# Kernel tuning notes

Measured on AMD Instinct MI355X. Metric: run time of the kernel, lower is better.

Reference implementation:

```python
import jax, jax.numpy as jnp
import numpy as np

ENTITY_TOTAL = 100000
RELATION_TOTAL = 500
NUM_RELATIONS = 2 * RELATION_TOTAL  # 1000
DIM = 128
NUM_BASES = 4
NUM_EDGES = 600000


def setup_inputs() -> dict:
    key = jax.random.key(0)
    ks = jax.random.split(key, 16)
    d = {}
    d['entity'] = jnp.arange(ENTITY_TOTAL, dtype=jnp.int64 if jax.config.jax_enable_x64 else jnp.int32)
    d['edge_index'] = jax.random.randint(ks[0], (2, NUM_EDGES), 0, ENTITY_TOTAL)
    d['edge_type'] = jax.random.randint(ks[1], (NUM_EDGES,), 0, NUM_RELATIONS)
    d['edge_norm'] = jax.random.uniform(ks[2], (NUM_EDGES,), dtype=jnp.float32)
    d['DAD_rel'] = jax.random.normal(ks[3], (RELATION_TOTAL, RELATION_TOTAL), dtype=jnp.float32)
    # learned parameters
    d['entity_table'] = jax.random.normal(ks[4], (ENTITY_TOTAL, DIM), dtype=jnp.float32)
    d['relation_emb'] = jax.random.normal(ks[5], (RELATION_TOTAL, DIM), dtype=jnp.float32) * (6.0 / (RELATION_TOTAL + DIM)) ** 0.5
    def rgcn_params(k):
        k1, k2, k3 = jax.random.split(k, 3)
        basis = jax.random.normal(k1, (NUM_BASES, DIM, DIM), dtype=jnp.float32) / np.sqrt(DIM)
        att = jax.random.normal(k2, (NUM_RELATIONS, NUM_BASES), dtype=jnp.float32) / np.sqrt(NUM_BASES)
        root = jax.random.normal(k3, (DIM, DIM), dtype=jnp.float32) / np.sqrt(DIM)
        bias = jnp.zeros((DIM,), dtype=jnp.float32)
        return basis, att, root, bias
    d['basis1'], d['att1'], d['root1'], d['bias1'] = rgcn_params(ks[6])
    d['basis2'], d['att2'], d['root2'], d['bias2'] = rgcn_params(ks[7])
    return d


def rgcn_conv(x, edge_index, edge_type, edge_norm, basis, att, root, bias):
    # PyG-style basis-decomposed RGCNConv, aggr='mean', source_to_target flow.
    num_nodes = x.shape[0]
    src, dst = edge_index[0], edge_index[1]
    x_j = x[src]                     # [E, in] gather
    att_e = att[edge_type]           # [E, B]
    # per-edge relation transform: sum_b att_e[:,b] * (x_j @ basis[b]); loop over
    # NUM_BASES (=4) avoids materializing [E, in, out].
    msg = jnp.zeros((x_j.shape[0], basis.shape[2]), dtype=x.dtype)
    for b in range(basis.shape[0]):
        msg = msg + att_e[:, b:b + 1] * (x_j @ basis[b])
    msg = msg * edge_norm[:, None]
    agg = jax.ops.segment_sum(msg, dst, num_segments=num_nodes)
    deg = jax.ops.segment_sum(jnp.ones_like(edge_norm), dst, num_segments=num_nodes)
    agg = agg / jnp.maximum(deg, 1.0)[:, None]   # mean aggregation
    return agg + x @ root + bias


def reference(entity, edge_index, edge_type, edge_norm, DAD_rel,
              entity_table, relation_emb,
              basis1, att1, root1, bias1,
              basis2, att2, root2, bias2):
    h = entity_table[entity]  # embedding lookup [N, dim]
    h = jax.nn.relu(rgcn_conv(h, edge_index, edge_type, edge_norm, basis1, att1, root1, bias1))
    # dropout(p=0.2) is identity in eval mode (deterministic reference)
    h = rgcn_conv(h, edge_index, edge_type, edge_norm, basis2, att2, root2, bias2)
    return (h, relation_emb)
```

## Files before the change

kernel.cpp:

```cpp
#include <hip/hip_runtime.h>
#include <hip/hip_bf16.h>

#define NROWS 100000
#define EDGES 600000
#define DIM 128
#define SCAN_B 391

typedef unsigned short u16;
typedef __attribute__((ext_vector_type(8))) short v8s;
typedef __attribute__((ext_vector_type(4))) float v4f;
typedef __attribute__((ext_vector_type(2))) float f2;

static __device__ __forceinline__ float bf2f(u16 u) {
  union { unsigned u; float f; } c;
  c.u = (unsigned)u << 16;
  return c.f;
}
static __device__ __forceinline__ u16 f2bf(float f) {
  union { float f; unsigned u; } c;
  c.f = f;
  unsigned r = c.u + 0x7fff + ((c.u >> 16) & 1);
  return (u16)(r >> 16);
}
static __device__ __forceinline__ f2 bfpair(unsigned v) {
  union { unsigned u[2]; f2 f; } c;
  c.u[0] = v << 16;
  c.u[1] = v & 0xffff0000u;
  return c.f;
}
static __device__ __forceinline__ long ld_idx(const void* p, long i, int is64) {
  return is64 ? (long)((const long long*)p)[i] : (long)((const int*)p)[i];
}
static __device__ __forceinline__ float ld_f(const int* flags, const void* p, long i) {
  return flags[0] ? ((const float*)p)[i] : bf2f(((const u16*)p)[i]);
}

__global__ __launch_bounds__(256) void detect_kernel(
    const u16* __restrict__ table, const void* __restrict__ entity,
    const void* __restrict__ ei, const void* __restrict__ et,
    int* __restrict__ flags) {
  int gid = blockIdx.x * 256 + threadIdx.x;
  const ushort4* t4 = (const ushort4*)table;
  ushort4 v = t4[gid];
  int cf = ((((v.x >> 7) & 0xFF) == 0xFF) ? 1 : 0) +
           ((((v.y >> 7) & 0xFF) == 0xFF) ? 1 : 0) +
           ((((v.z >> 7) & 0xFF) == 0xFF) ? 1 : 0) +
           ((((v.w >> 7) & 0xFF) == 0xFF) ? 1 : 0);
  int cei = 0, cet = 0;
  if (gid < 1024) {
    cei = (((const int*)ei)[2 * gid + 1] != 0) ? 1 : 0;
    cet = (((const int*)et)[2 * gid + 1] != 0) ? 1 : 0;
  }
  __shared__ int s_f, s_ei, s_et;
  if (threadIdx.x == 0) { s_f = 0; s_ei = 0; s_et = 0; }
  __syncthreads();
  if (cf) atomicAdd(&s_f, cf);
  if (cei) atomicAdd(&s_ei, cei);
  if (cet) atomicAdd(&s_et, cet);
  __syncthreads();
  if (threadIdx.x == 0) {
    if (s_f) atomicAdd(flags + 0, s_f);
    if (s_ei) atomicAdd(flags + 2, s_ei);
    if (s_et) atomicAdd(flags + 3, s_et);
  }
  if (gid == 0) flags[1] = (((const int*)entity)[1] == 0) ? 1 : 0;
}

__global__ __launch_bounds__(256) void prep_kernel(
    const int* __restrict__ flags,
    const void* __restrict__ basis0, const void* __restrict__ root0, u16* __restrict__ Wt0,
    const void* __restrict__ basis1, const void* __restrict__ root1, u16* __restrict__ Wt1,
    const void* __restrict__ att0, const void* __restrict__ att1,
    float* __restrict__ attf0, float* __restrict__ attf1,
    const void* __restrict__ bias0, const void* __restrict__ bias1,
    float* __restrict__ biasf0, float* __restrict__ biasf1,
    const void* __restrict__ rel, float* __restrict__ relout) {
  int i = blockIdx.x * 256 + threadIdx.x;
  if (i < 2 * 81920) {
    const void* basis = (i < 81920) ? basis0 : basis1;
    const void* root = (i < 81920) ? root0 : root1;
    u16* Wt = (i < 81920) ? Wt0 : Wt1;
    int j = (i < 81920) ? i : i - 81920;
    int n = j >> 7, k = j & 127;
    float v;
    if (n < 512) {
      int b = n >> 7, c = n & 127;
      v = ld_f(flags, basis, (long)b * DIM * DIM + (long)k * DIM + c);
    } else {
      v = ld_f(flags, root, (long)k * DIM + (n - 512));
    }
    Wt[j] = f2bf(v);
    return;
  }
  i -= 163840;
  if (i < 64000) { relout[i] = ld_f(flags, rel, i); return; }
  i -= 64000;
  if (i < 4000) { attf0[i] = ld_f(flags, att0, i); return; }
  i -= 4000;
  if (i < 4000) { attf1[i] = ld_f(flags, att1, i); return; }
  i -= 4000;
  if (i < 128) { biasf0[i] = ld_f(flags, bias0, i); return; }
  i -= 128;
  if (i < 128) biasf1[i] = ld_f(flags, bias1, i);
}
#define PREP_THREADS (163840 + 64000 + 4000 + 4000 + 128 + 128)

__global__ __launch_bounds__(256) void gather_kernel(const int* __restrict__ flags,
                                                     const void* __restrict__ entity,
                                                     const void* __restrict__ table,
                                                     u16* __restrict__ hbf) {
  int gid = blockIdx.x * 256 + threadIdx.x;
  int row = gid >> 5, c4 = (gid & 31) * 4;
  if (row >= NROWS) return;
  long src = ld_idx(entity, row, flags[1]);
  ushort4 o;
  if (flags[0]) {
    float4 a = *(const float4*)((const float*)table + src * DIM + c4);
    o = make_ushort4(f2bf(a.x), f2bf(a.y), f2bf(a.z), f2bf(a.w));
  } else {
    o = *(const ushort4*)((const u16*)table + src * DIM + c4);
  }
  *(ushort4*)(hbf + (long)row * DIM + c4) = o;
}

__global__ __launch_bounds__(256) void hist_kernel(const int* __restrict__ flags,
                                                   const void* __restrict__ ei,
                                                   int* __restrict__ cnt) {
  int e = blockIdx.x * 256 + threadIdx.x;
  if (e < EDGES) atomicAdd(cnt + ld_idx(ei, EDGES + e, flags[2] == 0), 1);
}

__global__ __launch_bounds__(256) void scan1_kernel(const int* __restrict__ cnt,
                                                    int* __restrict__ rowPtr,
                                                    int* __restrict__ bsum) {
  __shared__ int sh[256];
  int i = blockIdx.x * 256 + threadIdx.x;
  int v = (i < NROWS) ? cnt[i] : 0;
  sh[threadIdx.x] = v;
  __syncthreads();
#pragma unroll
  for (int off = 1; off < 256; off <<= 1) {
    int t = (threadIdx.x >= off) ? sh[threadIdx.x - off] : 0;
    __syncthreads();
    sh[threadIdx.x] += t;
    __syncthreads();
  }
  if (i < NROWS) rowPtr[i] = sh[threadIdx.x] - v;
  if (threadIdx.x == 255) bsum[blockIdx.x] = sh[255];
}

__global__ __launch_bounds__(512) void scan2_kernel(int* __restrict__ bsum,
                                                    int* __restrict__ bofs,
                                                    int* __restrict__ rowPtr) {
  __shared__ int sh[512];
  int v = (threadIdx.x < SCAN_B) ? bsum[threadIdx.x] : 0;
  sh[threadIdx.x] = v;
  __syncthreads();
#pragma unroll
  for (int off = 1; off < 512; off <<= 1) {
    int t = (threadIdx.x >= off) ? sh[threadIdx.x - off] : 0;
    __syncthreads();
    sh[threadIdx.x] += t;
    __syncthreads();
  }
  if (threadIdx.x < SCAN_B) bofs[threadIdx.x] = sh[threadIdx.x] - v;
  if (threadIdx.x == 511) rowPtr[NROWS] = sh[511];
}

__global__ __launch_bounds__(256) void scan3_kernel(int* __restrict__ rowPtr,
                                                    const int* __restrict__ bofs,
                                                    int* __restrict__ cursor) {
  int i = blockIdx.x * 256 + threadIdx.x;
  if (i >= NROWS) return;
  int r = rowPtr[i] + bofs[blockIdx.x];
  rowPtr[i] = r;
  cursor[i] = r;
}

__global__ __launch_bounds__(256) void scatter_kernel(const int* __restrict__ flags,
                                                      const void* __restrict__ ei,
                                                      const void* __restrict__ et,
                                                      const void* __restrict__ enorm,
                                                      int* __restrict__ cursor,
                                                      int2* __restrict__ csr8) {
  int e = blockIdx.x * 256 + threadIdx.x;
  if (e >= EDGES) return;
  int is64e = (flags[2] == 0), is64t = (flags[3] == 0);
  int dst = (int)ld_idx(ei, EDGES + e, is64e);
  int src = (int)ld_idx(ei, e, is64e);
  int t = (int)ld_idx(et, e, is64t);
  float nrm = ld_f(flags, enorm, e);
  int pos = atomicAdd(cursor + dst, 1);
  int2 v;
  v.x = src | (t << 17);
  v.y = __float_as_int(nrm);
  csr8[pos] = v;
}

__global__ __launch_bounds__(256) void zagg_kernel(
    const int* __restrict__ rowPtr, const int2* __restrict__ csr8,
    const float* __restrict__ att_f,
    const u16* __restrict__ hin, u16* __restrict__ Z, int c0, int c1) {
  int wid = (blockIdx.x * 256 + threadIdx.x) >> 6;
  int node = c0 + wid;
  if (node >= c1) return;
  int lane = threadIdx.x & 63, d = lane * 2;
  int beg = rowPtr[node], end = rowPtr[node + 1];
  const float4* att4 = (const float4*)att_f;
  f2 z0 = {0.f, 0.f}, z1 = {0.f, 0.f}, z2 = {0.f, 0.f}, z3 = {0.f, 0.f};
  int e = beg;
  for (; e + 1 < end; e += 2) {
    int2 p0 = csr8[e], p1 = csr8[e + 1];
    unsigned v0 = *(const unsigned*)(hin + (long)(p0.x & 0x1FFFF) * DIM + d);
    unsigned v1 = *(const unsigned*)(hin + (long)(p1.x & 0x1FFFF) * DIM + d);
    float4 a0 = att4[p0.x >> 17];
    float4 a1 = att4[p1.x >> 17];
    float n0 = __int_as_float(p0.y), n1 = __int_as_float(p1.y);
    f2 y0 = bfpair(v0) * (f2){n0, n0};
    f2 y1 = bfpair(v1) * (f2){n1, n1};
    z0 = (f2){a0.x, a0.x} * y0 + z0;
    z1 = (f2){a0.y, a0.y} * y0 + z1;
    z2 = (f2){a0.z, a0.z} * y0 + z2;
    z3 = (f2){a0.w, a0.w} * y0 + z3;
    z0 = (f2){a1.x, a1.x} * y1 + z0;
    z1 = (f2){a1.y, a1.y} * y1 + z1;
    z2 = (f2){a1.z, a1.z} * y1 + z2;
    z3 = (f2){a1.w, a1.w} * y1 + z3;
  }
  if (e < end) {
    int2 p0 = csr8[e];
    unsigned v0 = *(const unsigned*)(hin + (long)(p0.x & 0x1FFFF) * DIM + d);
    float4 a0 = att4[p0.x >> 17];
    float n0 = __int_as_float(p0.y);
    f2 y0 = bfpair(v0) * (f2){n0, n0};
    z0 = (f2){a0.x, a0.x} * y0 + z0;
    z1 = (f2){a0.y, a0.y} * y0 + z1;
    z2 = (f2){a0.z, a0.z} * y0 + z2;
    z3 = (f2){a0.w, a0.w} * y0 + z3;
  }
  float invd = 1.0f / fmaxf((float)(end - beg), 1.0f);
  f2 iv = {invd, invd};
  z0 *= iv; z1 *= iv; z2 *= iv; z3 *= iv;
  unsigned* zp = (unsigned*)(Z + (long)(node - c0) * 512) + lane;
  zp[0]   = (unsigned)f2bf(z0[0]) | ((unsigned)f2bf(z0[1]) << 16);
  zp[64]  = (unsigned)f2bf(z1[0]) | ((unsigned)f2bf(z1[1]) << 16);
  zp[128] = (unsigned)f2bf(z2[0]) | ((unsigned)f2bf(z2[1]) << 16);
  zp[192] = (unsigned)f2bf(z3[0]) | ((unsigned)f2bf(z3[1]) << 16);
}

__global__ __launch_bounds__(256) void fgemm_kernel(
    const u16* __restrict__ Z, const u16* __restrict__ hin,
    const u16* __restrict__ Wt, const float* __restrict__ bias,
    int c0, int c1, int finalMode,
    u16* __restrict__ hout, float* __restrict__ outp) {
  __shared__ u16 Wl[128 * 136];
  int wave = threadIdx.x >> 6, lane = threadIdx.x & 63;
  int quad = lane >> 4, l16 = lane & 15;
  long lrow = (long)blockIdx.x * 64 + wave * 16 + l16;
  long arow = c0 + lrow;
  bool rv = arow < c1;

  v4f av[8];
#pragma unroll
  for (int nt = 0; nt < 8; ++nt) av[nt] = (v4f){0.f, 0.f, 0.f, 0.f};

  for (int seg = 0; seg < 5; ++seg) {
#pragma unroll
    for (int it = 0; it < 8; ++it) {
      int idx = threadIdx.x + it * 256;
      int n = idx >> 4, kk = (idx & 15) * 8;
      *(int4*)&Wl[n * 136 + kk] = *(const int4*)&Wt[(long)(seg * 128 + n) * 128 + kk];
    }
    __syncthreads();
    const u16* abase = (seg < 4) ? Z + lrow * 512 + seg * 128
                                 : hin + arow * 128;
#pragma unroll
    for (int ks = 0; ks < 4; ++ks) {
      int k0 = ks * 32;
      v8s a = {0, 0, 0, 0, 0, 0, 0, 0};
      if (rv) a = *(const v8s*)&abase[k0 + quad * 8];
#pragma unroll
      for (int nt = 0; nt < 8; ++nt) {
        v8s b = *(const v8s*)&Wl[(nt * 16 + l16) * 136 + k0 + quad * 8];
        av[nt] = __builtin_amdgcn_mfma_f32_16x16x32_bf16(a, b, av[nt], 0, 0, 0);
      }
    }
    __syncthreads();
  }

  long orow0 = c0 + (long)blockIdx.x * 64 + wave * 16 + quad * 4;
#pragma unroll
  for (int nt = 0; nt < 8; ++nt) {
    int col = nt * 16 + l16;
    float bv = bias[col];
#pragma unroll
    for (int r = 0; r < 4; ++r) {
      long row = orow0 + r;
      if (row >= c1) continue;
      float v = av[nt][r] + bv;
      if (finalMode == 1) hout[row * DIM + col] = f2bf(fmaxf(v, 0.f));
      else                outp[row * DIM + col] = v;
    }
  }
}

static size_t alignup(size_t x) { return (x + 255) & ~(size_t)255; }

extern "C" void kernel_launch(void* const* d_in, const int* in_sizes, int n_in,
                              void* d_out, int out_size, void* d_ws, size_t ws_size,
                              hipStream_t stream) {
  static const long exp_sz[15] = {100000, 1200000, 600000, 600000, 250000,
                                  12800000, 64000, 65536, 4000, 16384, 128,
                                  65536, 4000, 16384, 128};
  int map[15];
  bool posOK = (n_in >= 15);
  for (int i = 0; posOK && i < 15; ++i) posOK = (in_sizes[i] == exp_sz[i]);
  if (posOK) {
    for (int i = 0; i < 15; ++i) map[i] = i;
  } else {
    bool used[64] = {};
    for (int i = 0; i < 15; ++i) {
      map[i] = -1;
      for (int j = 0; j < n_in && j < 64; ++j)
        if (!used[j] && in_sizes[j] == exp_sz[i]) { map[i] = j; used[j] = true; break; }
      if (map[i] < 0) map[i] = (i < n_in) ? i : 0;
    }
  }
  const void* entity = d_in[map[0]];
  const void* edge_index = d_in[map[1]];
  const void* edge_type = d_in[map[2]];
  const void* edge_norm = d_in[map[3]];
  const void* table = d_in[map[5]];
  const void* rel_emb = d_in[map[6]];
  const void* basis[2] = {d_in[map[7]], d_in[map[11]]};
  const void* att[2] = {d_in[map[8]], d_in[map[12]]};
  const void* root[2] = {d_in[map[9]], d_in[map[13]]};
  const void* bias[2] = {d_in[map[10]], d_in[map[14]]};

  char* ws = (char*)d_ws;
  size_t off = 0;
  auto grab = [&](size_t bytes) { size_t o = off; off = alignup(off + bytes); return o; };
  int* flags = (int*)(ws + grab(16));
  float* att_f[2] = {(float*)(ws + grab(4000 * 4)), (float*)(ws + grab(4000 * 4))};
  float* bias_f[2] = {(float*)(ws + grab(DIM * 4)), (float*)(ws + grab(DIM * 4))};
  u16* Wt[2] = {(u16*)(ws + grab(640 * 128 * 2)), (u16*)(ws + grab(640 * 128 * 2))};
  int* cnt = (int*)(ws + grab((size_t)NROWS * 4));
  int* cursor = (int*)(ws + grab((size_t)NROWS * 4));
  int* rowPtr = (int*)(ws + grab((size_t)(NROWS + 1) * 4));
  int* bsum = (int*)(ws + grab((size_t)SCAN_B * 4));
  int* bofs = (int*)(ws + grab((size_t)SCAN_B * 4));
  int2* csr8 = (int2*)(ws + grab((size_t)EDGES * 8));
  u16* hbf = (u16*)(ws + grab((size_t)NROWS * DIM * 2));
  u16* hbf2 = (u16*)(ws + grab((size_t)NROWS * DIM * 2));
  size_t fixedB = off;

  static const int ncOrd[5] = {1, 2, 4, 8, 16};
  int NC = 16;
  for (int i = 0; i < 5; ++i) {
    int nc = ncOrd[i];
    size_t r = (NROWS + nc - 1) / nc;
    if (fixedB + alignup(r * 512 * 2) <= ws_size) { NC = nc; break; }
  }
  const int rpc = (NROWS + NC - 1) / NC;
  u16* Z = (u16*)(ws + grab((size_t)rpc * 512 * 2));

  hipMemsetAsync(flags, 0, 16, stream);
  hipMemsetAsync(cnt, 0, (size_t)NROWS * 4, stream);
  detect_kernel<<<64, 256, 0, stream>>>((const u16*)table, entity, edge_index,
                                        edge_type, flags);
  prep_kernel<<<(PREP_THREADS + 255) / 256, 256, 0, stream>>>(
      flags, basis[0], root[0], Wt[0], basis[1], root[1], Wt[1],
      att[0], att[1], att_f[0], att_f[1],
      bias[0], bias[1], bias_f[0], bias_f[1],
      rel_emb, (float*)d_out + (size_t)NROWS * DIM);
  gather_kernel<<<(NROWS * 32 + 255) / 256, 256, 0, stream>>>(flags, entity, table, hbf);
  hist_kernel<<<(EDGES + 255) / 256, 256, 0, stream>>>(flags, edge_index, cnt);
  scan1_kernel<<<SCAN_B, 256, 0, stream>>>(cnt, rowPtr, bsum);
  scan2_kernel<<<1, 512, 0, stream>>>(bsum, bofs, rowPtr);
  scan3_kernel<<<SCAN_B, 256, 0, stream>>>(rowPtr, bofs, cursor);
  scatter_kernel<<<(EDGES + 255) / 256, 256, 0, stream>>>(
      flags, edge_index, edge_type, edge_norm, cursor, csr8);

  const u16* hin = hbf;
  for (int l = 0; l < 2; ++l) {
    for (int c = 0; c < NC; ++c) {
      int c0 = c * rpc, c1 = (c0 + rpc < NROWS) ? c0 + rpc : NROWS;
      int rc = c1 - c0;
      zagg_kernel<<<(rc * 64 + 255) / 256, 256, 0, stream>>>(
          rowPtr, csr8, att_f[l], hin, Z, c0, c1);
      fgemm_kernel<<<(rc + 63) / 64, 256, 0, stream>>>(
          Z, hin, Wt[l], bias_f[l], c0, c1, (l == 0) ? 1 : 2, hbf2, (float*)d_out);
    }
    hin = hbf2;
  }
}
```

Before: 430.4 us.

## Process two nodes per wave in aggregation and split GEMM columns across waves

The aggregation kernel now has each wave handle two destination nodes at once, interleaving their edge loops so twice as many independent gathers are in flight. The fused GEMM moves to 512-thread blocks where each pair of waves splits the 128 output columns, halving accumulators per wave. The weights are pre-permuted in the prep kernel into an MFMA-friendly layout, so the shared-memory fill becomes a flat copy and B-fragment reads become contiguous. The costs are imbalance when paired nodes differ in degree, and more register pressure in the aggregation kernel.

```diff
diff --git a/kernel.cpp b/kernel.cpp
--- a/kernel.cpp
+++ b/kernel.cpp
@@ -81,7 +81,13 @@
     const void* root = (i < 81920) ? root0 : root1;
     u16* Wt = (i < 81920) ? Wt0 : Wt1;
     int j = (i < 81920) ? i : i - 81920;
-    int n = j >> 7, k = j & 127;
+    int seg = j >> 14;
+    int r = j & 16383;
+    int kq = r >> 10;
+    int col = (r >> 3) & 127;
+    int w = r & 7;
+    int k = kq * 8 + w;
+    int n = seg * 128 + col;
     float v;
     if (n < 512) {
       int b = n >> 7, c = n & 127;
@@ -197,101 +203,163 @@
   csr8[pos] = v;
 }
 
+static __device__ __forceinline__ void edge1(int2 p0, const u16* __restrict__ hin,
+                                             int d, const float4* __restrict__ att4,
+                                             f2& z0, f2& z1, f2& z2, f2& z3) {
+  unsigned v0 = *(const unsigned*)(hin + (long)(p0.x & 0x1FFFF) * DIM + d);
+  float4 a0 = att4[p0.x >> 17];
+  float n0 = __int_as_float(p0.y);
+  f2 y0 = bfpair(v0) * (f2){n0, n0};
+  z0 = (f2){a0.x, a0.x} * y0 + z0;
+  z1 = (f2){a0.y, a0.y} * y0 + z1;
+  z2 = (f2){a0.z, a0.z} * y0 + z2;
+  z3 = (f2){a0.w, a0.w} * y0 + z3;
+}
+static __device__ __forceinline__ void edge2(int2 p0, int2 p1, const u16* __restrict__ hin,
+                                             int d, const float4* __restrict__ att4,
+                                             f2& z0, f2& z1, f2& z2, f2& z3) {
+  unsigned v0 = *(const unsigned*)(hin + (long)(p0.x & 0x1FFFF) * DIM + d);
+  unsigned v1 = *(const unsigned*)(hin + (long)(p1.x & 0x1FFFF) * DIM + d);
+  float4 a0 = att4[p0.x >> 17];
+  float4 a1 = att4[p1.x >> 17];
+  float n0 = __int_as_float(p0.y), n1 = __int_as_float(p1.y);
+  f2 y0 = bfpair(v0) * (f2){n0, n0};
+  f2 y1 = bfpair(v1) * (f2){n1, n1};
+  z0 = (f2){a0.x, a0.x} * y0 + z0;
+  z1 = (f2){a0.y, a0.y} * y0 + z1;
+  z2 = (f2){a0.z, a0.z} * y0 + z2;
+  z3 = (f2){a0.w, a0.w} * y0 + z3;
+  z0 = (f2){a1.x, a1.x} * y1 + z0;
+  z1 = (f2){a1.y, a1.y} * y1 + z1;
+  z2 = (f2){a1.z, a1.z} * y1 + z2;
+  z3 = (f2){a1.w, a1.w} * y1 + z3;
+}
+static __device__ __forceinline__ void zstore(u16* __restrict__ Z, long lrow, int lane,
+                                              f2 z0, f2 z1, f2 z2, f2 z3, float invd) {
+  f2 iv = {invd, invd};
+  z0 *= iv; z1 *= iv; z2 *= iv; z3 *= iv;
+  unsigned* zp = (unsigned*)(Z + lrow * 512) + lane;
+  zp[0]   = (unsigned)f2bf(z0[0]) | ((unsigned)f2bf(z0[1]) << 16);
+  zp[64]  = (unsigned)f2bf(z1[0]) | ((unsigned)f2bf(z1[1]) << 16);
+  zp[128] = (unsigned)f2bf(z2[0]) | ((unsigned)f2bf(z2[1]) << 16);
+  zp[192] = (unsigned)f2bf(z3[0]) | ((unsigned)f2bf(z3[1]) << 16);
+}
+
 __global__ __launch_bounds__(256) void zagg_kernel(
     const int* __restrict__ rowPtr, const int2* __restrict__ csr8,
     const float* __restrict__ att_f,
     const u16* __restrict__ hin, u16* __restrict__ Z, int c0, int c1) {
   int wid = (blockIdx.x * 256 + threadIdx.x) >> 6;
-  int node = c0 + wid;
-  if (node >= c1) return;
+  int rc = c1 - c0;
+  int half = (rc + 1) >> 1;
+  if (wid >= half) return;
+  int nA = c0 + wid, nB = nA + half;
+  bool hasB = nB < c1;
   int lane = threadIdx.x & 63, d = lane * 2;
-  int beg = rowPtr[node], end = rowPtr[node + 1];
   const float4* att4 = (const float4*)att_f;
-  f2 z0 = {0.f, 0.f}, z1 = {0.f, 0.f}, z2 = {0.f, 0.f}, z3 = {0.f, 0.f};
-  int e = beg;
-  for (; e + 1 < end; e += 2) {
-    int2 p0 = csr8[e], p1 = csr8[e + 1];
-    unsigned v0 = *(const unsigned*)(hin + (long)(p0.x & 0x1FFFF) * DIM + d);
-    unsigned v1 = *(const unsigned*)(hin + (long)(p1.x & 0x1FFFF) * DIM + d);
-    float4 a0 = att4[p0.x >> 17];
-    float4 a1 = att4[p1.x >> 17];
-    float n0 = __int_as_float(p0.y), n1 = __int_as_float(p1.y);
-    f2 y0 = bfpair(v0) * (f2){n0, n0};
-    f2 y1 = bfpair(v1) * (f2){n1, n1};
-    z0 = (f2){a0.x, a0.x} * y0 + z0;
-    z1 = (f2){a0.y, a0.y} * y0 + z1;
-    z2 = (f2){a0.z, a0.z} * y0 + z2;
-    z3 = (f2){a0.w, a0.w} * y0 + z3;
-    z0 = (f2){a1.x, a1.x} * y1 + z0;
-    z1 = (f2){a1.y, a1.y} * y1 + z1;
-    z2 = (f2){a1.z, a1.z} * y1 + z2;
-    z3 = (f2){a1.w, a1.w} * y1 + z3;
-  }
-  if (e < end) {
-    int2 p0 = csr8[e];
-    unsigned v0 = *(const unsigned*)(hin + (long)(p0.x & 0x1FFFF) * DIM + d);
-    float4 a0 = att4[p0.x >> 17];
-    float n0 = __int_as_float(p0.y);
-    f2 y0 = bfpair(v0) * (f2){n0, n0};
-    z0 = (f2){a0.x, a0.x} * y0 + z0;
-    z1 = (f2){a0.y, a0.y} * y0 + z1;
-    z2 = (f2){a0.z, a0.z} * y0 + z2;
-    z3 = (f2){a0.w, a0.w} * y0 + z3;
-  }
-  float invd = 1.0f / fmaxf((float)(end - beg), 1.0f);
-  f2 iv = {invd, invd};
-  z0 *= iv; z1 *= iv; z2 *= iv; z3 *= iv;
-  unsigned* zp = (unsigned*)(Z + (long)(node - c0) * 512) + lane;
-  zp[0]   = (unsigned)f2bf(z0[0]) | ((unsigned)f2bf(z0[1]) << 16);
-  zp[64]  = (unsigned)f2bf(z1[0]) | ((unsigned)f2bf(z1[1]) << 16);
-  zp[128] = (unsigned)f2bf(z2[0]) | ((unsigned)f2bf(z2[1]) << 16);
-  zp[192] = (unsigned)f2bf(z3[0]) | ((unsigned)f2bf(z3[1]) << 16);
-}
-
-__global__ __launch_bounds__(256) void fgemm_kernel(
+
+  int eA = rowPtr[nA], endA = rowPtr[nA + 1];
+  int eB = 0, endB = 0;
+  if (hasB) { eB = rowPtr[nB]; endB = rowPtr[nB + 1]; }
+  int begA = eA, begB = eB;
+
+  f2 zA0 = {0.f, 0.f}, zA1 = {0.f, 0.f}, zA2 = {0.f, 0.f}, zA3 = {0.f, 0.f};
+  f2 zB0 = {0.f, 0.f}, zB1 = {0.f, 0.f}, zB2 = {0.f, 0.f}, zB3 = {0.f, 0.f};
+
+  while (eA + 1 < endA && eB + 1 < endB) {
+    int2 pa0 = csr8[eA], pa1 = csr8[eA + 1];
+    int2 pb0 = csr8[eB], pb1 = csr8[eB + 1];
+    unsigned va0 = *(const unsigned*)(hin + (long)(pa0.x & 0x1FFFF) * DIM + d);
+    unsigned va1 = *(const unsigned*)(hin + (long)(pa1.x & 0x1FFFF) * DIM + d);
+    unsigned vb0 = *(const unsigned*)(hin + (long)(pb0.x & 0x1FFFF) * DIM + d);
+    unsigned vb1 = *(const unsigned*)(hin + (long)(pb1.x & 0x1FFFF) * DIM + d);
+    float4 aa0 = att4[pa0.x >> 17];
+    float4 aa1 = att4[pa1.x >> 17];
+    float4 ab0 = att4[pb0.x >> 17];
+    float4 ab1 = att4[pb1.x >> 17];
+    float na0 = __int_as_float(pa0.y), na1 = __int_as_float(pa1.y);
+    float nb0 = __int_as_float(pb0.y), nb1 = __int_as_float(pb1.y);
+    f2 ya0 = bfpair(va0) * (f2){na0, na0};
+    f2 ya1 = bfpair(va1) * (f2){na1, na1};
+    f2 yb0 = bfpair(vb0) * (f2){nb0, nb0};
+    f2 yb1 = bfpair(vb1) * (f2){nb1, nb1};
+    zA0 = (f2){aa0.x, aa0.x} * ya0 + zA0;
+    zA1 = (f2){aa0.y, aa0.y} * ya0 + zA1;
+    zA2 = (f2){aa0.z, aa0.z} * ya0 + zA2;
+    zA3 = (f2){aa0.w, aa0.w} * ya0 + zA3;
+    zA0 = (f2){aa1.x, aa1.x} * ya1 + zA0;
+    zA1 = (f2){aa1.y, aa1.y} * ya1 + zA1;
+    zA2 = (f2){aa1.z, aa1.z} * ya1 + zA2;
+    zA3 = (f2){aa1.w, aa1.w} * ya1 + zA3;
+    zB0 = (f2){ab0.x, ab0.x} * yb0 + zB0;
+    zB1 = (f2){ab0.y, ab0.y} * yb0 + zB1;
+    zB2 = (f2){ab0.z, ab0.z} * yb0 + zB2;
+    zB3 = (f2){ab0.w, ab0.w} * yb0 + zB3;
+    zB0 = (f2){ab1.x, ab1.x} * yb1 + zB0;
+    zB1 = (f2){ab1.y, ab1.y} * yb1 + zB1;
+    zB2 = (f2){ab1.z, ab1.z} * yb1 + zB2;
+    zB3 = (f2){ab1.w, ab1.w} * yb1 + zB3;
+    eA += 2; eB += 2;
+  }
+  for (; eA + 1 < endA; eA += 2)
+    edge2(csr8[eA], csr8[eA + 1], hin, d, att4, zA0, zA1, zA2, zA3);
+  if (eA < endA) edge1(csr8[eA], hin, d, att4, zA0, zA1, zA2, zA3);
+  for (; eB + 1 < endB; eB += 2)
+    edge2(csr8[eB], csr8[eB + 1], hin, d, att4, zB0, zB1, zB2, zB3);
+  if (eB < endB) edge1(csr8[eB], hin, d, att4, zB0, zB1, zB2, zB3);
+
+  zstore(Z, (long)(nA - c0), lane, zA0, zA1, zA2, zA3,
+         1.0f / fmaxf((float)(endA - begA), 1.0f));
+  if (hasB)
+    zstore(Z, (long)(nB - c0), lane, zB0, zB1, zB2, zB3,
+           1.0f / fmaxf((float)(endB - begB), 1.0f));
+}
+
+__global__ __launch_bounds__(512) void fgemm_kernel(
     const u16* __restrict__ Z, const u16* __restrict__ hin,
     const u16* __restrict__ Wt, const float* __restrict__ bias,
     int c0, int c1, int finalMode,
     u16* __restrict__ hout, float* __restrict__ outp) {
-  __shared__ u16 Wl[128 * 136];
-  int wave = threadIdx.x >> 6, lane = threadIdx.x & 63;
+  __shared__ u16 Wl[16384];
+  int tid = threadIdx.x;
+  int wv = tid >> 6, lane = tid & 63;
+  int rt = wv >> 1, ch = wv & 1;
   int quad = lane >> 4, l16 = lane & 15;
-  long lrow = (long)blockIdx.x * 64 + wave * 16 + l16;
+  long lrow = (long)blockIdx.x * 64 + rt * 16 + l16;
   long arow = c0 + lrow;
   bool rv = arow < c1;
 
-  v4f av[8];
-#pragma unroll
-  for (int nt = 0; nt < 8; ++nt) av[nt] = (v4f){0.f, 0.f, 0.f, 0.f};
+  v4f av[4];
+#pragma unroll
+  for (int nt = 0; nt < 4; ++nt) av[nt] = (v4f){0.f, 0.f, 0.f, 0.f};
 
   for (int seg = 0; seg < 5; ++seg) {
-#pragma unroll
-    for (int it = 0; it < 8; ++it) {
-      int idx = threadIdx.x + it * 256;
-      int n = idx >> 4, kk = (idx & 15) * 8;
-      *(int4*)&Wl[n * 136 + kk] = *(const int4*)&Wt[(long)(seg * 128 + n) * 128 + kk];
+    if (seg) __syncthreads();
+#pragma unroll
+    for (int it = 0; it < 4; ++it) {
+      int o = (tid + it * 512) * 8;
+      *(int4*)&Wl[o] = *(const int4*)&Wt[(long)seg * 16384 + o];
     }
     __syncthreads();
     const u16* abase = (seg < 4) ? Z + lrow * 512 + seg * 128
                                  : hin + arow * 128;
 #pragma unroll
     for (int ks = 0; ks < 4; ++ks) {
-      int k0 = ks * 32;
       v8s a = {0, 0, 0, 0, 0, 0, 0, 0};
-      if (rv) a = *(const v8s*)&abase[k0 + quad * 8];
-#pragma unroll
-      for (int nt = 0; nt < 8; ++nt) {
-        v8s b = *(const v8s*)&Wl[(nt * 16 + l16) * 136 + k0 + quad * 8];
+      if (rv) a = *(const v8s*)&abase[ks * 32 + quad * 8];
+      const u16* wb = &Wl[(ks * 4 + quad) * 1024 + ch * 512];
+#pragma unroll
+      for (int nt = 0; nt < 4; ++nt) {
+        v8s b = *(const v8s*)&wb[(nt * 16 + l16) * 8];
         av[nt] = __builtin_amdgcn_mfma_f32_16x16x32_bf16(a, b, av[nt], 0, 0, 0);
       }
     }
-    __syncthreads();
-  }
-
-  long orow0 = c0 + (long)blockIdx.x * 64 + wave * 16 + quad * 4;
-#pragma unroll
-  for (int nt = 0; nt < 8; ++nt) {
-    int col = nt * 16 + l16;
+  }
+
+  long orow0 = c0 + (long)blockIdx.x * 64 + rt * 16 + quad * 4;
+#pragma unroll
+  for (int nt = 0; nt < 4; ++nt) {
+    int col = ch * 64 + nt * 16 + l16;
     float bv = bias[col];
 #pragma unroll
     for (int r = 0; r < 4; ++r) {
@@ -386,9 +454,10 @@
     for (int c = 0; c < NC; ++c) {
       int c0 = c * rpc, c1 = (c0 + rpc < NROWS) ? c0 + rpc : NROWS;
       int rc = c1 - c0;
-      zagg_kernel<<<(rc * 64 + 255) / 256, 256, 0, stream>>>(
+      int halfw = (rc + 1) / 2;
+      zagg_kernel<<<(halfw * 64 + 255) / 256, 256, 0, stream>>>(
           rowPtr, csr8, att_f[l], hin, Z, c0, c1);
-      fgemm_kernel<<<(rc + 63) / 64, 256, 0, stream>>>(
+      fgemm_kernel<<<(rc + 63) / 64, 512, 0, stream>>>(
           Z, hin, Wt[l], bias_f[l], c0, c1, (l == 0) ? 1 : 2, hbf2, (float*)d_out);
     }
     hin = hbf2;
```

Result: no change. 428.2 us (-0.5%).
